# Optimization experiments

Hardware: AMD Instinct MI355X
Metric: run time of the kernel (lower is better)

Reference implementation:

```python
import jax, jax.numpy as jnp
import numpy as np

B, IN_DIM, UNITS, NUM_K, NUM_S = 4096, 128, 256, 64, 256


def setup_inputs() -> dict:
    key = jax.random.key(0)
    ks = jax.random.split(key, 24)
    d = {
        "X": jax.random.normal(ks[0], (B, IN_DIM), jnp.float32),
        "h_prev": jax.random.normal(ks[1], (B, UNITS), jnp.float32),
        "c_prev": jax.random.normal(ks[2], (B, UNITS), jnp.float32),
        "M_prev": jax.random.normal(ks[3], (B, NUM_K, NUM_S), jnp.float32),
        "k_prev": jax.random.normal(ks[4], (B, NUM_S), jnp.float32),
    }
    rows = IN_DIM + UNITS
    s = 0.05
    d["Wf"] = jax.random.normal(ks[5], (rows, UNITS), jnp.float32) * s
    d["Wt"] = jax.random.normal(ks[6], (rows, UNITS), jnp.float32) * s
    d["Wi"] = jax.random.normal(ks[7], (rows, UNITS), jnp.float32) * s
    d["Wo"] = jax.random.normal(ks[8], (rows, UNITS), jnp.float32) * s
    d["bf"] = jnp.zeros((UNITS,), jnp.float32)
    d["bt"] = jnp.zeros((UNITS,), jnp.float32)
    d["bi"] = jnp.zeros((UNITS,), jnp.float32)
    d["bo"] = jnp.zeros((UNITS,), jnp.float32)
    d["Wk"] = jax.random.normal(ks[9], (UNITS, NUM_S), jnp.float32) * s
    d["bk"] = jnp.zeros((NUM_S,), jnp.float32)
    d["Wr"] = jax.random.normal(ks[10], (NUM_S, UNITS), jnp.float32) * s
    d["Wc"] = jax.random.normal(ks[11], (UNITS, UNITS), jnp.float32) * s
    d["Wh"] = jax.random.normal(ks[12], (NUM_S, UNITS), jnp.float32) * s
    d["We"] = jax.random.normal(ks[13], (UNITS, NUM_S), jnp.float32) * s
    d["be"] = jnp.zeros((NUM_S,), jnp.float32)
    d["Wa"] = jax.random.normal(ks[14], (UNITS, NUM_S), jnp.float32) * s
    d["ba"] = jnp.zeros((NUM_S,), jnp.float32)
    return d


def _l2n(x):
    # matches tf.nn.l2_normalize: x / sqrt(max(sum(x^2), eps))
    return x / jnp.sqrt(jnp.maximum(jnp.sum(x * x, axis=-1, keepdims=True), 1e-12))


def reference(X, h_prev, c_prev, M_prev, k_prev,
              Wf, Wt, Wi, Wo, bf, bt, bi, bo,
              Wk, bk, Wr, Wc, Wh, We, be, Wa, ba):
    sig = jax.nn.sigmoid
    xh = jnp.concatenate([X, h_prev], axis=-1)          # (B, in+units)
    i = sig(xh @ Wi + bi)
    f = sig(xh @ Wf + bf)
    o = sig(xh @ Wo + bo)
    t = sig(xh @ Wt + bt)
    c = f * c_prev + i * t                              # (B, units)

    # tf.keras.losses.cosine_similarity returns NEGATIVE cosine similarity
    cos = jnp.einsum('bks,bs->bk', _l2n(M_prev), _l2n(k_prev))
    alpha = jax.nn.softmax(-cos, axis=-1)               # (B, K)
    r = jnp.einsum('bk,bks->bs', alpha, M_prev)         # content read (B, S)

    rc_1 = sig(r @ Wr + c @ Wc)
    h_curr = o * jnp.tanh(c + rc_1 * (r @ Wh))          # (B, units)

    k_curr = jnp.tanh(h_curr @ Wk + bk)                 # (B, S)
    e = sig(h_curr @ We + be)                           # erase  (B, S)
    a = jnp.tanh(h_curr @ Wa + ba)                      # add    (B, S)
    al = alpha[:, :, None]                              # (B, K, 1)
    M_curr = M_prev * (1.0 - al * e[:, None, :]) + al * a[:, None, :]
    return h_curr, c, M_curr, k_curr
```

## Files before the change

### kernel.cpp

```cpp
#include <hip/hip_runtime.h>
#include <math.h>


#define BATCH 4096
#define INDIM 128
#define UNITS 256
#define NUMK  64
#define NUMS  256

__device__ __forceinline__ float sigf(float x) { return 1.0f / (1.0f + expf(-x)); }

__global__ __launch_bounds__(256) void k1_gates(
    const float* __restrict__ X, const float* __restrict__ h_prev,
    const float* __restrict__ c_prev,
    const float* __restrict__ Wf, const float* __restrict__ Wt,
    const float* __restrict__ Wi, const float* __restrict__ Wo,
    const float* __restrict__ bf, const float* __restrict__ bt,
    const float* __restrict__ bi, const float* __restrict__ bo,
    float* __restrict__ c_out, float* __restrict__ o_out)
{
    __shared__ float sA[16][68];
    __shared__ float sB[4][16][68];

    const int t  = threadIdx.x;
    const int bm = blockIdx.x;
    const int bn = blockIdx.y;

    float acc[4][4][4];
    #pragma unroll
    for (int g = 0; g < 4; ++g)
        #pragma unroll
        for (int mi = 0; mi < 4; ++mi)
            #pragma unroll
            for (int ni = 0; ni < 4; ++ni) acc[g][mi][ni] = 0.0f;

    const float* Wg[4] = {Wf, Wt, Wi, Wo};

    const int m0 = (t & 15) * 4;
    const int n0 = (t >> 4) * 4;
    const int lm  = t >> 2;
    const int lk  = (t & 3) * 4;
    const int lbk = t >> 4;
    const int lbc = (t & 15) * 4;

    for (int k0 = 0; k0 < 384; k0 += 16) {
        {
            const int row = bm * 64 + lm;
            const int gk = k0 + lk;
            float4 av;
            if (gk < INDIM) av = *(const float4*)(X + row * INDIM + gk);
            else            av = *(const float4*)(h_prev + row * UNITS + (gk - INDIM));
            sA[lk + 0][lm] = av.x; sA[lk + 1][lm] = av.y;
            sA[lk + 2][lm] = av.z; sA[lk + 3][lm] = av.w;
        }
        #pragma unroll
        for (int g = 0; g < 4; ++g) {
            float4 bv = *(const float4*)(Wg[g] + (k0 + lbk) * UNITS + bn * 64 + lbc);
            *(float4*)&sB[g][lbk][lbc] = bv;
        }
        __syncthreads();
        #pragma unroll
        for (int k = 0; k < 16; ++k) {
            float a[4];
            *(float4*)a = *(float4*)&sA[k][m0];
            #pragma unroll
            for (int g = 0; g < 4; ++g) {
                float b[4];
                *(float4*)b = *(float4*)&sB[g][k][n0];
                #pragma unroll
                for (int mi = 0; mi < 4; ++mi)
                    #pragma unroll
                    for (int ni = 0; ni < 4; ++ni)
                        acc[g][mi][ni] = fmaf(a[mi], b[ni], acc[g][mi][ni]);
            }
        }
        __syncthreads();
    }

    const int col0 = bn * 64 + n0;
    const int row0 = bm * 64 + m0;
    float bfv[4], btv[4], biv[4], bov[4];
    *(float4*)bfv = *(const float4*)(bf + col0);
    *(float4*)btv = *(const float4*)(bt + col0);
    *(float4*)biv = *(const float4*)(bi + col0);
    *(float4*)bov = *(const float4*)(bo + col0);
    #pragma unroll
    for (int mi = 0; mi < 4; ++mi) {
        const int row = row0 + mi;
        float cp[4];
        *(float4*)cp = *(const float4*)(c_prev + row * UNITS + col0);
        float cv[4], ov[4];
        #pragma unroll
        for (int ni = 0; ni < 4; ++ni) {
            float fv = sigf(acc[0][mi][ni] + bfv[ni]);
            float tv = sigf(acc[1][mi][ni] + btv[ni]);
            float iv = sigf(acc[2][mi][ni] + biv[ni]);
            float oo = sigf(acc[3][mi][ni] + bov[ni]);
            cv[ni] = fv * cp[ni] + iv * tv;
            ov[ni] = oo;
        }
        *(float4*)(c_out + row * UNITS + col0) = *(float4*)cv;
        *(float4*)(o_out + row * UNITS + col0) = *(float4*)ov;
    }
}

__global__ __launch_bounds__(256) void k2_cosr(
    const float* __restrict__ M, const float* __restrict__ k_prev,
    float* __restrict__ alpha_out, float* __restrict__ r_out)
{
    const int b = blockIdx.x;
    const int t = threadIdx.x;
    const int lane = t & 63;
    const int w = t >> 6;

    __shared__ float scos[64];
    __shared__ float salpha[64];
    __shared__ float spr[4][256];

    const float4 k4 = *(const float4*)(k_prev + b * NUMS + lane * 4);
    float kss = k4.x * k4.x + k4.y * k4.y + k4.z * k4.z + k4.w * k4.w;
    #pragma unroll
    for (int m = 1; m < 64; m <<= 1) kss += __shfl_xor(kss, m, 64);
    const float knorm = sqrtf(fmaxf(kss, 1e-12f));

    const float* Mb = M + (size_t)b * (NUMK * NUMS);
    float4 mreg[16];
    #pragma unroll
    for (int j = 0; j < 16; ++j)
        mreg[j] = *(const float4*)(Mb + (w * 16 + j) * NUMS + lane * 4);

    #pragma unroll
    for (int j = 0; j < 16; ++j) {
        const float4 m4 = mreg[j];
        float dot = m4.x * k4.x + m4.y * k4.y + m4.z * k4.z + m4.w * k4.w;
        float ssq = m4.x * m4.x + m4.y * m4.y + m4.z * m4.z + m4.w * m4.w;
        #pragma unroll
        for (int m = 1; m < 64; m <<= 1) {
            dot += __shfl_xor(dot, m, 64);
            ssq += __shfl_xor(ssq, m, 64);
        }
        if (lane == 0) {
            const float mnorm = sqrtf(fmaxf(ssq, 1e-12f));
            scos[w * 16 + j] = dot / (mnorm * knorm);
        }
    }
    __syncthreads();

    if (t < 64) {
        float v = -scos[t];
        float vmax = v;
        #pragma unroll
        for (int m = 1; m < 64; m <<= 1) vmax = fmaxf(vmax, __shfl_xor(vmax, m, 64));
        float e = expf(v - vmax);
        float s = e;
        #pragma unroll
        for (int m = 1; m < 64; m <<= 1) s += __shfl_xor(s, m, 64);
        const float al = e / s;
        salpha[t] = al;
        alpha_out[b * NUMK + t] = al;
    }
    __syncthreads();

    float pr0 = 0.f, pr1 = 0.f, pr2 = 0.f, pr3 = 0.f;
    #pragma unroll
    for (int j = 0; j < 16; ++j) {
        const float al = salpha[w * 16 + j];
        pr0 = fmaf(al, mreg[j].x, pr0);
        pr1 = fmaf(al, mreg[j].y, pr1);
        pr2 = fmaf(al, mreg[j].z, pr2);
        pr3 = fmaf(al, mreg[j].w, pr3);
    }
    *(float4*)&spr[w][lane * 4] = make_float4(pr0, pr1, pr2, pr3);
    __syncthreads();
    const float rv = spr[0][t] + spr[1][t] + spr[2][t] + spr[3][t];
    r_out[b * NUMS + t] = rv;
}

__global__ __launch_bounds__(256) void k3_h(
    const float* __restrict__ r, const float* __restrict__ c,
    const float* __restrict__ o,
    const float* __restrict__ Wr, const float* __restrict__ Wc,
    const float* __restrict__ Wh,
    float* __restrict__ h_out)
{
    __shared__ float sAr[16][68];
    __shared__ float sAc[16][68];
    __shared__ float sB[3][16][68];

    const int t  = threadIdx.x;
    const int bm = blockIdx.x;
    const int bn = blockIdx.y;

    float acc[3][4][4];
    #pragma unroll
    for (int g = 0; g < 3; ++g)
        #pragma unroll
        for (int mi = 0; mi < 4; ++mi)
            #pragma unroll
            for (int ni = 0; ni < 4; ++ni) acc[g][mi][ni] = 0.0f;

    const float* Wg[3] = {Wr, Wc, Wh};
    const int m0 = (t & 15) * 4;
    const int n0 = (t >> 4) * 4;
    const int lm  = t >> 2;
    const int lk  = (t & 3) * 4;
    const int lbk = t >> 4;
    const int lbc = (t & 15) * 4;

    for (int k0 = 0; k0 < 256; k0 += 16) {
        {
            const int row = bm * 64 + lm;
            float4 rv = *(const float4*)(r + row * UNITS + k0 + lk);
            float4 cv = *(const float4*)(c + row * UNITS + k0 + lk);
            sAr[lk + 0][lm] = rv.x; sAr[lk + 1][lm] = rv.y;
            sAr[lk + 2][lm] = rv.z; sAr[lk + 3][lm] = rv.w;
            sAc[lk + 0][lm] = cv.x; sAc[lk + 1][lm] = cv.y;
            sAc[lk + 2][lm] = cv.z; sAc[lk + 3][lm] = cv.w;
        }
        #pragma unroll
        for (int g = 0; g < 3; ++g) {
            float4 bv = *(const float4*)(Wg[g] + (k0 + lbk) * UNITS + bn * 64 + lbc);
            *(float4*)&sB[g][lbk][lbc] = bv;
        }
        __syncthreads();
        #pragma unroll
        for (int k = 0; k < 16; ++k) {
            float ar[4], ac[4];
            *(float4*)ar = *(float4*)&sAr[k][m0];
            *(float4*)ac = *(float4*)&sAc[k][m0];
            float b0[4], b1[4], b2[4];
            *(float4*)b0 = *(float4*)&sB[0][k][n0];
            *(float4*)b1 = *(float4*)&sB[1][k][n0];
            *(float4*)b2 = *(float4*)&sB[2][k][n0];
            #pragma unroll
            for (int mi = 0; mi < 4; ++mi)
                #pragma unroll
                for (int ni = 0; ni < 4; ++ni) {
                    acc[0][mi][ni] = fmaf(ar[mi], b0[ni], acc[0][mi][ni]);
                    acc[1][mi][ni] = fmaf(ac[mi], b1[ni], acc[1][mi][ni]);
                    acc[2][mi][ni] = fmaf(ar[mi], b2[ni], acc[2][mi][ni]);
                }
        }
        __syncthreads();
    }

    const int col0 = bn * 64 + n0;
    const int row0 = bm * 64 + m0;
    #pragma unroll
    for (int mi = 0; mi < 4; ++mi) {
        const int row = row0 + mi;
        float cv[4], ov[4], hv[4];
        *(float4*)cv = *(const float4*)(c + row * UNITS + col0);
        *(float4*)ov = *(const float4*)(o + row * UNITS + col0);
        #pragma unroll
        for (int ni = 0; ni < 4; ++ni) {
            const float rc1 = sigf(acc[0][mi][ni] + acc[1][mi][ni]);
            hv[ni] = ov[ni] * tanhf(cv[ni] + rc1 * acc[2][mi][ni]);
        }
        *(float4*)(h_out + row * UNITS + col0) = *(float4*)hv;
    }
}

__global__ __launch_bounds__(256) void k4_kea(
    const float* __restrict__ h,
    const float* __restrict__ Wk, const float* __restrict__ We,
    const float* __restrict__ Wa,
    const float* __restrict__ bk, const float* __restrict__ be,
    const float* __restrict__ ba,
    float* __restrict__ k_out, float* __restrict__ e_out, float* __restrict__ a_out)
{
    __shared__ float sA[16][68];
    __shared__ float sB[3][16][68];

    const int t  = threadIdx.x;
    const int bm = blockIdx.x;
    const int bn = blockIdx.y;

    float acc[3][4][4];
    #pragma unroll
    for (int g = 0; g < 3; ++g)
        #pragma unroll
        for (int mi = 0; mi < 4; ++mi)
            #pragma unroll
            for (int ni = 0; ni < 4; ++ni) acc[g][mi][ni] = 0.0f;

    const float* Wg[3] = {Wk, We, Wa};
    const int m0 = (t & 15) * 4;
    const int n0 = (t >> 4) * 4;
    const int lm  = t >> 2;
    const int lk  = (t & 3) * 4;
    const int lbk = t >> 4;
    const int lbc = (t & 15) * 4;

    for (int k0 = 0; k0 < 256; k0 += 16) {
        {
            const int row = bm * 64 + lm;
            float4 av = *(const float4*)(h + row * UNITS + k0 + lk);
            sA[lk + 0][lm] = av.x; sA[lk + 1][lm] = av.y;
            sA[lk + 2][lm] = av.z; sA[lk + 3][lm] = av.w;
        }
        #pragma unroll
        for (int g = 0; g < 3; ++g) {
            float4 bv = *(const float4*)(Wg[g] + (k0 + lbk) * UNITS + bn * 64 + lbc);
            *(float4*)&sB[g][lbk][lbc] = bv;
        }
        __syncthreads();
        #pragma unroll
        for (int k = 0; k < 16; ++k) {
            float a[4];
            *(float4*)a = *(float4*)&sA[k][m0];
            float b0[4], b1[4], b2[4];
            *(float4*)b0 = *(float4*)&sB[0][k][n0];
            *(float4*)b1 = *(float4*)&sB[1][k][n0];
            *(float4*)b2 = *(float4*)&sB[2][k][n0];
            #pragma unroll
            for (int mi = 0; mi < 4; ++mi)
                #pragma unroll
                for (int ni = 0; ni < 4; ++ni) {
                    acc[0][mi][ni] = fmaf(a[mi], b0[ni], acc[0][mi][ni]);
                    acc[1][mi][ni] = fmaf(a[mi], b1[ni], acc[1][mi][ni]);
                    acc[2][mi][ni] = fmaf(a[mi], b2[ni], acc[2][mi][ni]);
                }
        }
        __syncthreads();
    }

    const int col0 = bn * 64 + n0;
    const int row0 = bm * 64 + m0;
    float bkv[4], bev[4], bav[4];
    *(float4*)bkv = *(const float4*)(bk + col0);
    *(float4*)bev = *(const float4*)(be + col0);
    *(float4*)bav = *(const float4*)(ba + col0);
    #pragma unroll
    for (int mi = 0; mi < 4; ++mi) {
        const int row = row0 + mi;
        float kv[4], ev[4], av[4];
        #pragma unroll
        for (int ni = 0; ni < 4; ++ni) {
            kv[ni] = tanhf(acc[0][mi][ni] + bkv[ni]);
            ev[ni] = sigf (acc[1][mi][ni] + bev[ni]);
            av[ni] = tanhf(acc[2][mi][ni] + bav[ni]);
        }
        *(float4*)(k_out + row * UNITS + col0) = *(float4*)kv;
        *(float4*)(e_out + row * UNITS + col0) = *(float4*)ev;
        *(float4*)(a_out + row * UNITS + col0) = *(float4*)av;
    }
}

__global__ __launch_bounds__(256) void k5_mup(
    const float* __restrict__ M, const float* __restrict__ alpha,
    const float* __restrict__ e, const float* __restrict__ a,
    float* __restrict__ Mout)
{
    const int b = blockIdx.x;
    const int t = threadIdx.x;
    __shared__ float sal[64];
    if (t < 64) sal[t] = alpha[b * NUMK + t];

    const int s4 = (t & 63) * 4;
    const int kr = t >> 6;
    const float4 e4 = *(const float4*)(e + b * NUMS + s4);
    const float4 a4 = *(const float4*)(a + b * NUMS + s4);
    __syncthreads();

    const float* Mb = M + (size_t)b * (NUMK * NUMS);
    float* Ob = Mout + (size_t)b * (NUMK * NUMS);
    #pragma unroll
    for (int j = 0; j < 16; ++j) {
        const int k = j * 4 + kr;
        const float al = sal[k];
        float4 m4 = *(const float4*)(Mb + k * NUMS + s4);
        float4 o4;
        o4.x = m4.x * (1.0f - al * e4.x) + al * a4.x;
        o4.y = m4.y * (1.0f - al * e4.y) + al * a4.y;
        o4.z = m4.z * (1.0f - al * e4.z) + al * a4.z;
        o4.w = m4.w * (1.0f - al * e4.w) + al * a4.w;
        *(float4*)(Ob + k * NUMS + s4) = o4;
    }
}

extern "C" void kernel_launch(void* const* d_in, const int* in_sizes, int n_in,
                              void* d_out, int out_size, void* d_ws, size_t ws_size,
                              hipStream_t stream)
{
    (void)in_sizes; (void)n_in; (void)out_size; (void)ws_size;

    const float* X      = (const float*)d_in[0];
    const float* h_prev = (const float*)d_in[1];
    const float* c_prev = (const float*)d_in[2];
    const float* M_prev = (const float*)d_in[3];
    const float* k_prev = (const float*)d_in[4];
    const float* Wf = (const float*)d_in[5];
    const float* Wt = (const float*)d_in[6];
    const float* Wi = (const float*)d_in[7];
    const float* Wo = (const float*)d_in[8];
    const float* bf = (const float*)d_in[9];
    const float* bt = (const float*)d_in[10];
    const float* bi = (const float*)d_in[11];
    const float* bo = (const float*)d_in[12];
    const float* Wk = (const float*)d_in[13];
    const float* bk = (const float*)d_in[14];
    const float* Wr = (const float*)d_in[15];
    const float* Wc = (const float*)d_in[16];
    const float* Wh = (const float*)d_in[17];
    const float* We = (const float*)d_in[18];
    const float* be = (const float*)d_in[19];
    const float* Wa = (const float*)d_in[20];
    const float* ba = (const float*)d_in[21];

    float* out = (float*)d_out;
    float* h_out = out;
    float* c_out = out + 1048576;
    float* M_out = out + 2097152;
    float* k_out = out + 69206016;

    float* ws    = (float*)d_ws;
    float* o_ws  = ws;
    float* al_ws = ws + 1048576;
    float* r_ws  = ws + 1310720;
    float* e_ws  = ws + 2359296;
    float* a_ws  = ws + 3407872;

    k1_gates<<<dim3(64, 4), 256, 0, stream>>>(X, h_prev, c_prev,
                                              Wf, Wt, Wi, Wo, bf, bt, bi, bo,
                                              c_out, o_ws);
    k2_cosr<<<dim3(4096), 256, 0, stream>>>(M_prev, k_prev, al_ws, r_ws);
    k3_h<<<dim3(64, 4), 256, 0, stream>>>(r_ws, c_out, o_ws, Wr, Wc, Wh, h_out);
    k4_kea<<<dim3(64, 4), 256, 0, stream>>>(h_out, Wk, We, Wa, bk, be, ba,
                                            k_out, e_ws, a_ws);
    k5_mup<<<dim3(4096), 256, 0, stream>>>(M_prev, al_ws, e_ws, a_ws, M_out);
}
```

Measured before the change: 720.7 us.

## Replace FP32 SIMT GEMMs with split-bf16 MFMA GEMMs plus elementwise epilogues

Replaces the three shared-memory FP32 FMA GEMM kernels with a generic MFMA GEMM that emulates FP32 precision using hi/lo bf16 splits (three MFMAs per tile). Weights and activations are packed into transposed bf16 hi/lo buffers by new pack and prep kernels, and gate nonlinearities move into separate elementwise kernels that also emit the next GEMM's split operands. The cosine reduction now uses partial shuffles plus shared-memory sums, and the large M reads and writes use nontemporal loads and stores. The cost is extra launches, weight repacking on every call, and large intermediate buffers written to and read back from global memory.

```diff
diff --git a/kernel.cpp b/kernel.cpp
--- a/kernel.cpp
+++ b/kernel.cpp
@@ -8,112 +8,208 @@
 #define NUMK  64
 #define NUMS  256
 
+typedef unsigned short u16;
+typedef __attribute__((ext_vector_type(4))) float  f32x4;
+typedef __attribute__((ext_vector_type(8))) short  s16x8;
+typedef __attribute__((ext_vector_type(4))) u16    u16x4;
+typedef __attribute__((ext_vector_type(8))) u16    u16x8;
+
 __device__ __forceinline__ float sigf(float x) { return 1.0f / (1.0f + expf(-x)); }
 
-__global__ __launch_bounds__(256) void k1_gates(
-    const float* __restrict__ X, const float* __restrict__ h_prev,
-    const float* __restrict__ c_prev,
+__device__ __forceinline__ u16 f2bf(float x) {
+    unsigned u = __float_as_uint(x);
+    return (u16)((u + 0x7fffu + ((u >> 16) & 1u)) >> 16);
+}
+__device__ __forceinline__ float bf2f(u16 h) {
+    return __uint_as_float(((unsigned)h) << 16);
+}
+__device__ __forceinline__ void split_bf(float x, u16& hi, u16& lo) {
+    hi = f2bf(x);
+    lo = f2bf(x - bf2f(hi));
+}
+
+__global__ __launch_bounds__(256) void prep_a1(
+    const float* __restrict__ X, const float* __restrict__ hp,
+    u16* __restrict__ Ahi, u16* __restrict__ Alo)
+{
+    const int idx = blockIdx.x * 256 + threadIdx.x;
+    const int row = idx / 96;
+    const int cg  = (idx - row * 96) * 4;
+    float4 v;
+    if (cg < INDIM) v = *(const float4*)(X + row * INDIM + cg);
+    else            v = *(const float4*)(hp + row * UNITS + (cg - INDIM));
+    u16x4 h, l;
+    u16 th, tl;
+    split_bf(v.x, th, tl); h.x = th; l.x = tl;
+    split_bf(v.y, th, tl); h.y = th; l.y = tl;
+    split_bf(v.z, th, tl); h.z = th; l.z = tl;
+    split_bf(v.w, th, tl); h.w = th; l.w = tl;
+    *(u16x4*)(Ahi + row * 384 + cg) = h;
+    *(u16x4*)(Alo + row * 384 + cg) = l;
+}
+
+__global__ __launch_bounds__(256) void pack_w1(
     const float* __restrict__ Wf, const float* __restrict__ Wt,
     const float* __restrict__ Wi, const float* __restrict__ Wo,
+    u16* __restrict__ Whi, u16* __restrict__ Wlo)
+{
+    const int tid = blockIdx.x * 256 + threadIdx.x;
+    const int n  = tid / 48;
+    const int k0 = (tid - n * 48) * 8;
+    const float* src = (n < 256) ? Wf : (n < 512) ? Wt : (n < 768) ? Wi : Wo;
+    const int nc = n & 255;
+    u16x8 h, l;
+    #pragma unroll
+    for (int j = 0; j < 8; ++j) {
+        float x = src[(k0 + j) * 256 + nc];
+        u16 th, tl;
+        split_bf(x, th, tl);
+        h[j] = th; l[j] = tl;
+    }
+    *(u16x8*)(Whi + n * 384 + k0) = h;
+    *(u16x8*)(Wlo + n * 384 + k0) = l;
+}
+
+__global__ __launch_bounds__(256) void pack_w3(
+    const float* __restrict__ Wr, const float* __restrict__ Wc,
+    const float* __restrict__ Wh,
+    u16* __restrict__ Whi, u16* __restrict__ Wlo)
+{
+    const int tid = blockIdx.x * 256 + threadIdx.x;
+    const int n  = tid / 64;
+    const int k0 = (tid - n * 64) * 8;
+    u16x8 h, l;
+    #pragma unroll
+    for (int j = 0; j < 8; ++j) {
+        const int k = k0 + j;
+        float x;
+        if (n < 256) x = (k < 256) ? Wr[k * 256 + n] : Wc[(k - 256) * 256 + n];
+        else         x = (k < 256) ? Wh[k * 256 + (n - 256)] : 0.0f;
+        u16 th, tl;
+        split_bf(x, th, tl);
+        h[j] = th; l[j] = tl;
+    }
+    *(u16x8*)(Whi + n * 512 + k0) = h;
+    *(u16x8*)(Wlo + n * 512 + k0) = l;
+}
+
+__global__ __launch_bounds__(256) void pack_w4(
+    const float* __restrict__ Wk, const float* __restrict__ We,
+    const float* __restrict__ Wa,
+    u16* __restrict__ Whi, u16* __restrict__ Wlo)
+{
+    const int tid = blockIdx.x * 256 + threadIdx.x;
+    const int n  = tid / 32;
+    const int k0 = (tid - n * 32) * 8;
+    const float* src = (n < 256) ? Wk : (n < 512) ? We : Wa;
+    const int nc = n & 255;
+    u16x8 h, l;
+    #pragma unroll
+    for (int j = 0; j < 8; ++j) {
+        float x = src[(k0 + j) * 256 + nc];
+        u16 th, tl;
+        split_bf(x, th, tl);
+        h[j] = th; l[j] = tl;
+    }
+    *(u16x8*)(Whi + n * 256 + k0) = h;
+    *(u16x8*)(Wlo + n * 256 + k0) = l;
+}
+
+template<int K>
+__global__ __launch_bounds__(256) void gemm_bf16x2(
+    const u16* __restrict__ Ahi, const u16* __restrict__ Alo,
+    const u16* __restrict__ Bhi, const u16* __restrict__ Blo,
+    float* __restrict__ C, int N)
+{
+    const int t = threadIdx.x;
+    const int wave = t >> 6, lane = t & 63;
+    const int m0 = blockIdx.x * 64 + wave * 16;
+    const int n0 = blockIdx.y * 64;
+    const int r = lane & 15, g = lane >> 4;
+
+    const u16* pAh = Ahi + (size_t)(m0 + r) * K + g * 8;
+    const u16* pAl = Alo + (size_t)(m0 + r) * K + g * 8;
+    const u16* pBh = Bhi + (size_t)(n0 + r) * K + g * 8;
+    const u16* pBl = Blo + (size_t)(n0 + r) * K + g * 8;
+
+    f32x4 acc[4];
+    #pragma unroll
+    for (int j = 0; j < 4; ++j) acc[j] = (f32x4){0.f, 0.f, 0.f, 0.f};
+
+    #pragma unroll 2
+    for (int k0 = 0; k0 < K; k0 += 32) {
+        s16x8 ah = *(const s16x8*)(pAh + k0);
+        s16x8 al = *(const s16x8*)(pAl + k0);
+        #pragma unroll
+        for (int j = 0; j < 4; ++j) {
+            s16x8 bh = *(const s16x8*)(pBh + (size_t)j * 16 * K + k0);
+            s16x8 bl = *(const s16x8*)(pBl + (size_t)j * 16 * K + k0);
+            acc[j] = __builtin_amdgcn_mfma_f32_16x16x32_bf16(ah, bh, acc[j], 0, 0, 0);
+            acc[j] = __builtin_amdgcn_mfma_f32_16x16x32_bf16(al, bh, acc[j], 0, 0, 0);
+            acc[j] = __builtin_amdgcn_mfma_f32_16x16x32_bf16(ah, bl, acc[j], 0, 0, 0);
+        }
+    }
+
+    #pragma unroll
+    for (int j = 0; j < 4; ++j)
+        #pragma unroll
+        for (int rr = 0; rr < 4; ++rr)
+            C[(size_t)(m0 + g * 4 + rr) * N + (n0 + j * 16 + r)] = acc[j][rr];
+}
+
+__global__ __launch_bounds__(256) void e1(
+    const float* __restrict__ G1, const float* __restrict__ c_prev,
     const float* __restrict__ bf, const float* __restrict__ bt,
     const float* __restrict__ bi, const float* __restrict__ bo,
-    float* __restrict__ c_out, float* __restrict__ o_out)
-{
-    __shared__ float sA[16][68];
-    __shared__ float sB[4][16][68];
-
-    const int t  = threadIdx.x;
-    const int bm = blockIdx.x;
-    const int bn = blockIdx.y;
-
-    float acc[4][4][4];
-    #pragma unroll
-    for (int g = 0; g < 4; ++g)
-        #pragma unroll
-        for (int mi = 0; mi < 4; ++mi)
-            #pragma unroll
-            for (int ni = 0; ni < 4; ++ni) acc[g][mi][ni] = 0.0f;
-
-    const float* Wg[4] = {Wf, Wt, Wi, Wo};
-
-    const int m0 = (t & 15) * 4;
-    const int n0 = (t >> 4) * 4;
-    const int lm  = t >> 2;
-    const int lk  = (t & 3) * 4;
-    const int lbk = t >> 4;
-    const int lbc = (t & 15) * 4;
-
-    for (int k0 = 0; k0 < 384; k0 += 16) {
-        {
-            const int row = bm * 64 + lm;
-            const int gk = k0 + lk;
-            float4 av;
-            if (gk < INDIM) av = *(const float4*)(X + row * INDIM + gk);
-            else            av = *(const float4*)(h_prev + row * UNITS + (gk - INDIM));
-            sA[lk + 0][lm] = av.x; sA[lk + 1][lm] = av.y;
-            sA[lk + 2][lm] = av.z; sA[lk + 3][lm] = av.w;
-        }
-        #pragma unroll
-        for (int g = 0; g < 4; ++g) {
-            float4 bv = *(const float4*)(Wg[g] + (k0 + lbk) * UNITS + bn * 64 + lbc);
-            *(float4*)&sB[g][lbk][lbc] = bv;
-        }
-        __syncthreads();
-        #pragma unroll
-        for (int k = 0; k < 16; ++k) {
-            float a[4];
-            *(float4*)a = *(float4*)&sA[k][m0];
-            #pragma unroll
-            for (int g = 0; g < 4; ++g) {
-                float b[4];
-                *(float4*)b = *(float4*)&sB[g][k][n0];
-                #pragma unroll
-                for (int mi = 0; mi < 4; ++mi)
-                    #pragma unroll
-                    for (int ni = 0; ni < 4; ++ni)
-                        acc[g][mi][ni] = fmaf(a[mi], b[ni], acc[g][mi][ni]);
-            }
-        }
-        __syncthreads();
-    }
-
-    const int col0 = bn * 64 + n0;
-    const int row0 = bm * 64 + m0;
-    float bfv[4], btv[4], biv[4], bov[4];
-    *(float4*)bfv = *(const float4*)(bf + col0);
-    *(float4*)btv = *(const float4*)(bt + col0);
-    *(float4*)biv = *(const float4*)(bi + col0);
-    *(float4*)bov = *(const float4*)(bo + col0);
-    #pragma unroll
-    for (int mi = 0; mi < 4; ++mi) {
-        const int row = row0 + mi;
-        float cp[4];
-        *(float4*)cp = *(const float4*)(c_prev + row * UNITS + col0);
-        float cv[4], ov[4];
-        #pragma unroll
-        for (int ni = 0; ni < 4; ++ni) {
-            float fv = sigf(acc[0][mi][ni] + bfv[ni]);
-            float tv = sigf(acc[1][mi][ni] + btv[ni]);
-            float iv = sigf(acc[2][mi][ni] + biv[ni]);
-            float oo = sigf(acc[3][mi][ni] + bov[ni]);
-            cv[ni] = fv * cp[ni] + iv * tv;
-            ov[ni] = oo;
-        }
-        *(float4*)(c_out + row * UNITS + col0) = *(float4*)cv;
-        *(float4*)(o_out + row * UNITS + col0) = *(float4*)ov;
-    }
+    float* __restrict__ c_out, u16* __restrict__ A3hi, u16* __restrict__ A3lo,
+    float* __restrict__ o_ws)
+{
+    const int idx = blockIdx.x * 256 + threadIdx.x;
+    const int row = idx >> 6;
+    const int c0  = (idx & 63) * 4;
+    const float* g = G1 + (size_t)row * 1024 + c0;
+    float4 fv = *(const float4*)(g);
+    float4 tv = *(const float4*)(g + 256);
+    float4 iv = *(const float4*)(g + 512);
+    float4 ov = *(const float4*)(g + 768);
+    float4 bfv = *(const float4*)(bf + c0), btv = *(const float4*)(bt + c0);
+    float4 biv = *(const float4*)(bi + c0), bov = *(const float4*)(bo + c0);
+    float4 cp = *(const float4*)(c_prev + (size_t)row * 256 + c0);
+    float fa[4] = {fv.x, fv.y, fv.z, fv.w}, ta[4] = {tv.x, tv.y, tv.z, tv.w};
+    float ia[4] = {iv.x, iv.y, iv.z, iv.w}, oa[4] = {ov.x, ov.y, ov.z, ov.w};
+    float ba_f[4] = {bfv.x, bfv.y, bfv.z, bfv.w}, ba_t[4] = {btv.x, btv.y, btv.z, btv.w};
+    float ba_i[4] = {biv.x, biv.y, biv.z, biv.w}, ba_o[4] = {bov.x, bov.y, bov.z, bov.w};
+    float cpa[4] = {cp.x, cp.y, cp.z, cp.w};
+    float cv[4], oo[4];
+    u16x4 chi, clo;
+    #pragma unroll
+    for (int j = 0; j < 4; ++j) {
+        float f = sigf(fa[j] + ba_f[j]);
+        float tt = sigf(ta[j] + ba_t[j]);
+        float i = sigf(ia[j] + ba_i[j]);
+        oo[j] = sigf(oa[j] + ba_o[j]);
+        cv[j] = f * cpa[j] + i * tt;
+        u16 th, tl;
+        split_bf(cv[j], th, tl);
+        chi[j] = th; clo[j] = tl;
+    }
+    *(float4*)(c_out + (size_t)row * 256 + c0) = make_float4(cv[0], cv[1], cv[2], cv[3]);
+    *(float4*)(o_ws + (size_t)row * 256 + c0) = make_float4(oo[0], oo[1], oo[2], oo[3]);
+    *(u16x4*)(A3hi + (size_t)row * 512 + 256 + c0) = chi;
+    *(u16x4*)(A3lo + (size_t)row * 512 + 256 + c0) = clo;
 }
 
 __global__ __launch_bounds__(256) void k2_cosr(
     const float* __restrict__ M, const float* __restrict__ k_prev,
-    float* __restrict__ alpha_out, float* __restrict__ r_out)
+    float* __restrict__ alpha_out, u16* __restrict__ A3hi, u16* __restrict__ A3lo)
 {
     const int b = blockIdx.x;
     const int t = threadIdx.x;
     const int lane = t & 63;
     const int w = t >> 6;
 
-    __shared__ float scos[64];
+    __shared__ float sdot[64][8];
+    __shared__ float sssq[64][8];
     __shared__ float salpha[64];
     __shared__ float spr[4][256];
 
@@ -124,30 +220,34 @@
     const float knorm = sqrtf(fmaxf(kss, 1e-12f));
 
     const float* Mb = M + (size_t)b * (NUMK * NUMS);
-    float4 mreg[16];
+    f32x4 mreg[16];
     #pragma unroll
     for (int j = 0; j < 16; ++j)
-        mreg[j] = *(const float4*)(Mb + (w * 16 + j) * NUMS + lane * 4);
+        mreg[j] = __builtin_nontemporal_load((const f32x4*)(Mb + (w * 16 + j) * NUMS + lane * 4));
 
     #pragma unroll
     for (int j = 0; j < 16; ++j) {
-        const float4 m4 = mreg[j];
+        const f32x4 m4 = mreg[j];
         float dot = m4.x * k4.x + m4.y * k4.y + m4.z * k4.z + m4.w * k4.w;
         float ssq = m4.x * m4.x + m4.y * m4.y + m4.z * m4.z + m4.w * m4.w;
         #pragma unroll
-        for (int m = 1; m < 64; m <<= 1) {
+        for (int m = 1; m < 8; m <<= 1) {
             dot += __shfl_xor(dot, m, 64);
             ssq += __shfl_xor(ssq, m, 64);
         }
-        if (lane == 0) {
-            const float mnorm = sqrtf(fmaxf(ssq, 1e-12f));
-            scos[w * 16 + j] = dot / (mnorm * knorm);
+        if ((lane & 7) == 0) {
+            sdot[w * 16 + j][lane >> 3] = dot;
+            sssq[w * 16 + j][lane >> 3] = ssq;
         }
     }
     __syncthreads();
 
     if (t < 64) {
-        float v = -scos[t];
+        float dot = 0.f, ssq = 0.f;
+        #pragma unroll
+        for (int q = 0; q < 8; ++q) { dot += sdot[t][q]; ssq += sssq[t][q]; }
+        const float cosv = dot / (sqrtf(fmaxf(ssq, 1e-12f)) * knorm);
+        float v = -cosv;
         float vmax = v;
         #pragma unroll
         for (int m = 1; m < 64; m <<= 1) vmax = fmaxf(vmax, __shfl_xor(vmax, m, 64));
@@ -173,178 +273,69 @@
     *(float4*)&spr[w][lane * 4] = make_float4(pr0, pr1, pr2, pr3);
     __syncthreads();
     const float rv = spr[0][t] + spr[1][t] + spr[2][t] + spr[3][t];
-    r_out[b * NUMS + t] = rv;
-}
-
-__global__ __launch_bounds__(256) void k3_h(
-    const float* __restrict__ r, const float* __restrict__ c,
+    u16 hi, lo;
+    split_bf(rv, hi, lo);
+    A3hi[(size_t)b * 512 + t] = hi;
+    A3lo[(size_t)b * 512 + t] = lo;
+}
+
+__global__ __launch_bounds__(256) void e2(
+    const float* __restrict__ G3, const float* __restrict__ c,
     const float* __restrict__ o,
-    const float* __restrict__ Wr, const float* __restrict__ Wc,
-    const float* __restrict__ Wh,
-    float* __restrict__ h_out)
-{
-    __shared__ float sAr[16][68];
-    __shared__ float sAc[16][68];
-    __shared__ float sB[3][16][68];
-
-    const int t  = threadIdx.x;
-    const int bm = blockIdx.x;
-    const int bn = blockIdx.y;
-
-    float acc[3][4][4];
-    #pragma unroll
-    for (int g = 0; g < 3; ++g)
-        #pragma unroll
-        for (int mi = 0; mi < 4; ++mi)
-            #pragma unroll
-            for (int ni = 0; ni < 4; ++ni) acc[g][mi][ni] = 0.0f;
-
-    const float* Wg[3] = {Wr, Wc, Wh};
-    const int m0 = (t & 15) * 4;
-    const int n0 = (t >> 4) * 4;
-    const int lm  = t >> 2;
-    const int lk  = (t & 3) * 4;
-    const int lbk = t >> 4;
-    const int lbc = (t & 15) * 4;
-
-    for (int k0 = 0; k0 < 256; k0 += 16) {
-        {
-            const int row = bm * 64 + lm;
-            float4 rv = *(const float4*)(r + row * UNITS + k0 + lk);
-            float4 cv = *(const float4*)(c + row * UNITS + k0 + lk);
-            sAr[lk + 0][lm] = rv.x; sAr[lk + 1][lm] = rv.y;
-            sAr[lk + 2][lm] = rv.z; sAr[lk + 3][lm] = rv.w;
-            sAc[lk + 0][lm] = cv.x; sAc[lk + 1][lm] = cv.y;
-            sAc[lk + 2][lm] = cv.z; sAc[lk + 3][lm] = cv.w;
-        }
-        #pragma unroll
-        for (int g = 0; g < 3; ++g) {
-            float4 bv = *(const float4*)(Wg[g] + (k0 + lbk) * UNITS + bn * 64 + lbc);
-            *(float4*)&sB[g][lbk][lbc] = bv;
-        }
-        __syncthreads();
-        #pragma unroll
-        for (int k = 0; k < 16; ++k) {
-            float ar[4], ac[4];
-            *(float4*)ar = *(float4*)&sAr[k][m0];
-            *(float4*)ac = *(float4*)&sAc[k][m0];
-            float b0[4], b1[4], b2[4];
-            *(float4*)b0 = *(float4*)&sB[0][k][n0];
-            *(float4*)b1 = *(float4*)&sB[1][k][n0];
-            *(float4*)b2 = *(float4*)&sB[2][k][n0];
-            #pragma unroll
-            for (int mi = 0; mi < 4; ++mi)
-                #pragma unroll
-                for (int ni = 0; ni < 4; ++ni) {
-                    acc[0][mi][ni] = fmaf(ar[mi], b0[ni], acc[0][mi][ni]);
-                    acc[1][mi][ni] = fmaf(ac[mi], b1[ni], acc[1][mi][ni]);
-                    acc[2][mi][ni] = fmaf(ar[mi], b2[ni], acc[2][mi][ni]);
-                }
-        }
-        __syncthreads();
-    }
-
-    const int col0 = bn * 64 + n0;
-    const int row0 = bm * 64 + m0;
-    #pragma unroll
-    for (int mi = 0; mi < 4; ++mi) {
-        const int row = row0 + mi;
-        float cv[4], ov[4], hv[4];
-        *(float4*)cv = *(const float4*)(c + row * UNITS + col0);
-        *(float4*)ov = *(const float4*)(o + row * UNITS + col0);
-        #pragma unroll
-        for (int ni = 0; ni < 4; ++ni) {
-            const float rc1 = sigf(acc[0][mi][ni] + acc[1][mi][ni]);
-            hv[ni] = ov[ni] * tanhf(cv[ni] + rc1 * acc[2][mi][ni]);
-        }
-        *(float4*)(h_out + row * UNITS + col0) = *(float4*)hv;
-    }
-}
-
-__global__ __launch_bounds__(256) void k4_kea(
-    const float* __restrict__ h,
-    const float* __restrict__ Wk, const float* __restrict__ We,
-    const float* __restrict__ Wa,
+    float* __restrict__ h_out, u16* __restrict__ A4hi, u16* __restrict__ A4lo)
+{
+    const int idx = blockIdx.x * 256 + threadIdx.x;
+    const int row = idx >> 6;
+    const int c0  = (idx & 63) * 4;
+    float4 rc = *(const float4*)(G3 + (size_t)row * 512 + c0);
+    float4 rh = *(const float4*)(G3 + (size_t)row * 512 + 256 + c0);
+    float4 cv = *(const float4*)(c + (size_t)row * 256 + c0);
+    float4 ov = *(const float4*)(o + (size_t)row * 256 + c0);
+    float rca[4] = {rc.x, rc.y, rc.z, rc.w}, rha[4] = {rh.x, rh.y, rh.z, rh.w};
+    float ca[4] = {cv.x, cv.y, cv.z, cv.w}, oa[4] = {ov.x, ov.y, ov.z, ov.w};
+    float hv[4];
+    u16x4 hhi, hlo;
+    #pragma unroll
+    for (int j = 0; j < 4; ++j) {
+        hv[j] = oa[j] * tanhf(ca[j] + sigf(rca[j]) * rha[j]);
+        u16 th, tl;
+        split_bf(hv[j], th, tl);
+        hhi[j] = th; hlo[j] = tl;
+    }
+    *(float4*)(h_out + (size_t)row * 256 + c0) = make_float4(hv[0], hv[1], hv[2], hv[3]);
+    *(u16x4*)(A4hi + (size_t)row * 256 + c0) = hhi;
+    *(u16x4*)(A4lo + (size_t)row * 256 + c0) = hlo;
+}
+
+__global__ __launch_bounds__(256) void e3(
+    const float* __restrict__ G4,
     const float* __restrict__ bk, const float* __restrict__ be,
     const float* __restrict__ ba,
-    float* __restrict__ k_out, float* __restrict__ e_out, float* __restrict__ a_out)
-{
-    __shared__ float sA[16][68];
-    __shared__ float sB[3][16][68];
-
-    const int t  = threadIdx.x;
-    const int bm = blockIdx.x;
-    const int bn = blockIdx.y;
-
-    float acc[3][4][4];
-    #pragma unroll
-    for (int g = 0; g < 3; ++g)
-        #pragma unroll
-        for (int mi = 0; mi < 4; ++mi)
-            #pragma unroll
-            for (int ni = 0; ni < 4; ++ni) acc[g][mi][ni] = 0.0f;
-
-    const float* Wg[3] = {Wk, We, Wa};
-    const int m0 = (t & 15) * 4;
-    const int n0 = (t >> 4) * 4;
-    const int lm  = t >> 2;
-    const int lk  = (t & 3) * 4;
-    const int lbk = t >> 4;
-    const int lbc = (t & 15) * 4;
-
-    for (int k0 = 0; k0 < 256; k0 += 16) {
-        {
-            const int row = bm * 64 + lm;
-            float4 av = *(const float4*)(h + row * UNITS + k0 + lk);
-            sA[lk + 0][lm] = av.x; sA[lk + 1][lm] = av.y;
-            sA[lk + 2][lm] = av.z; sA[lk + 3][lm] = av.w;
-        }
-        #pragma unroll
-        for (int g = 0; g < 3; ++g) {
-            float4 bv = *(const float4*)(Wg[g] + (k0 + lbk) * UNITS + bn * 64 + lbc);
-            *(float4*)&sB[g][lbk][lbc] = bv;
-        }
-        __syncthreads();
-        #pragma unroll
-        for (int k = 0; k < 16; ++k) {
-            float a[4];
-            *(float4*)a = *(float4*)&sA[k][m0];
-            float b0[4], b1[4], b2[4];
-            *(float4*)b0 = *(float4*)&sB[0][k][n0];
-            *(float4*)b1 = *(float4*)&sB[1][k][n0];
-            *(float4*)b2 = *(float4*)&sB[2][k][n0];
-            #pragma unroll
-            for (int mi = 0; mi < 4; ++mi)
-                #pragma unroll
-                for (int ni = 0; ni < 4; ++ni) {
-                    acc[0][mi][ni] = fmaf(a[mi], b0[ni], acc[0][mi][ni]);
-                    acc[1][mi][ni] = fmaf(a[mi], b1[ni], acc[1][mi][ni]);
-                    acc[2][mi][ni] = fmaf(a[mi], b2[ni], acc[2][mi][ni]);
-                }
-        }
-        __syncthreads();
-    }
-
-    const int col0 = bn * 64 + n0;
-    const int row0 = bm * 64 + m0;
-    float bkv[4], bev[4], bav[4];
-    *(float4*)bkv = *(const float4*)(bk + col0);
-    *(float4*)bev = *(const float4*)(be + col0);
-    *(float4*)bav = *(const float4*)(ba + col0);
-    #pragma unroll
-    for (int mi = 0; mi < 4; ++mi) {
-        const int row = row0 + mi;
-        float kv[4], ev[4], av[4];
-        #pragma unroll
-        for (int ni = 0; ni < 4; ++ni) {
-            kv[ni] = tanhf(acc[0][mi][ni] + bkv[ni]);
-            ev[ni] = sigf (acc[1][mi][ni] + bev[ni]);
-            av[ni] = tanhf(acc[2][mi][ni] + bav[ni]);
-        }
-        *(float4*)(k_out + row * UNITS + col0) = *(float4*)kv;
-        *(float4*)(e_out + row * UNITS + col0) = *(float4*)ev;
-        *(float4*)(a_out + row * UNITS + col0) = *(float4*)av;
-    }
+    float* __restrict__ k_out, float* __restrict__ e_ws, float* __restrict__ a_ws)
+{
+    const int idx = blockIdx.x * 256 + threadIdx.x;
+    const int row = idx >> 6;
+    const int c0  = (idx & 63) * 4;
+    const float* g = G4 + (size_t)row * 768 + c0;
+    float4 kv = *(const float4*)(g);
+    float4 ev = *(const float4*)(g + 256);
+    float4 av = *(const float4*)(g + 512);
+    float4 bkv = *(const float4*)(bk + c0), bev = *(const float4*)(be + c0);
+    float4 bav = *(const float4*)(ba + c0);
+    float ka[4] = {kv.x, kv.y, kv.z, kv.w}, ea[4] = {ev.x, ev.y, ev.z, ev.w};
+    float aa[4] = {av.x, av.y, av.z, av.w};
+    float bka[4] = {bkv.x, bkv.y, bkv.z, bkv.w}, bea[4] = {bev.x, bev.y, bev.z, bev.w};
+    float baa[4] = {bav.x, bav.y, bav.z, bav.w};
+    float ko[4], eo[4], ao[4];
+    #pragma unroll
+    for (int j = 0; j < 4; ++j) {
+        ko[j] = tanhf(ka[j] + bka[j]);
+        eo[j] = sigf (ea[j] + bea[j]);
+        ao[j] = tanhf(aa[j] + baa[j]);
+    }
+    *(float4*)(k_out + (size_t)row * 256 + c0) = make_float4(ko[0], ko[1], ko[2], ko[3]);
+    *(float4*)(e_ws  + (size_t)row * 256 + c0) = make_float4(eo[0], eo[1], eo[2], eo[3]);
+    *(float4*)(a_ws  + (size_t)row * 256 + c0) = make_float4(ao[0], ao[1], ao[2], ao[3]);
 }
 
 __global__ __launch_bounds__(256) void k5_mup(
@@ -369,13 +360,13 @@
     for (int j = 0; j < 16; ++j) {
         const int k = j * 4 + kr;
         const float al = sal[k];
-        float4 m4 = *(const float4*)(Mb + k * NUMS + s4);
-        float4 o4;
+        f32x4 m4 = __builtin_nontemporal_load((const f32x4*)(Mb + k * NUMS + s4));
+        f32x4 o4;
         o4.x = m4.x * (1.0f - al * e4.x) + al * a4.x;
         o4.y = m4.y * (1.0f - al * e4.y) + al * a4.y;
         o4.z = m4.z * (1.0f - al * e4.z) + al * a4.z;
         o4.w = m4.w * (1.0f - al * e4.w) + al * a4.w;
-        *(float4*)(Ob + k * NUMS + s4) = o4;
+        __builtin_nontemporal_store(o4, (f32x4*)(Ob + k * NUMS + s4));
     }
 }
 
@@ -414,19 +405,44 @@
     float* M_out = out + 2097152;
     float* k_out = out + 69206016;
 
-    float* ws    = (float*)d_ws;
-    float* o_ws  = ws;
-    float* al_ws = ws + 1048576;
-    float* r_ws  = ws + 1310720;
-    float* e_ws  = ws + 2359296;
-    float* a_ws  = ws + 3407872;
-
-    k1_gates<<<dim3(64, 4), 256, 0, stream>>>(X, h_prev, c_prev,
-                                              Wf, Wt, Wi, Wo, bf, bt, bi, bo,
-                                              c_out, o_ws);
-    k2_cosr<<<dim3(4096), 256, 0, stream>>>(M_prev, k_prev, al_ws, r_ws);
-    k3_h<<<dim3(64, 4), 256, 0, stream>>>(r_ws, c_out, o_ws, Wr, Wc, Wh, h_out);
-    k4_kea<<<dim3(64, 4), 256, 0, stream>>>(h_out, Wk, We, Wa, bk, be, ba,
-                                            k_out, e_ws, a_ws);
-    k5_mup<<<dim3(4096), 256, 0, stream>>>(M_prev, al_ws, e_ws, a_ws, M_out);
-}
+    char* w = (char*)d_ws;
+    size_t off = 0;
+    auto carve = [&](size_t bytes) { void* p = w + off; off += (bytes + 255) & ~(size_t)255; return p; };
+    u16* A1hi = (u16*)carve(4096ull * 384 * 2);
+    u16* A1lo = (u16*)carve(4096ull * 384 * 2);
+    u16* W1hi = (u16*)carve(1024ull * 384 * 2);
+    u16* W1lo = (u16*)carve(1024ull * 384 * 2);
+    u16* W3hi = (u16*)carve(512ull * 512 * 2);
+    u16* W3lo = (u16*)carve(512ull * 512 * 2);
+    u16* W4hi = (u16*)carve(768ull * 256 * 2);
+    u16* W4lo = (u16*)carve(768ull * 256 * 2);
+    u16* A3hi = (u16*)carve(4096ull * 512 * 2);
+    u16* A3lo = (u16*)carve(4096ull * 512 * 2);
+    u16* A4hi = (u16*)carve(4096ull * 256 * 2);
+    u16* A4lo = (u16*)carve(4096ull * 256 * 2);
+    float* G1  = (float*)carve(4096ull * 1024 * 4);
+    float* G3  = (float*)carve(4096ull * 512 * 4);
+    float* G4  = (float*)carve(4096ull * 768 * 4);
+    float* o_ws  = (float*)carve(4096ull * 256 * 4);
+    float* al_ws = (float*)carve(4096ull * 64 * 4);
+    float* e_ws  = (float*)carve(4096ull * 256 * 4);
+    float* a_ws  = (float*)carve(4096ull * 256 * 4);
+
+    pack_w1<<<192, 256, 0, stream>>>(Wf, Wt, Wi, Wo, W1hi, W1lo);
+    pack_w3<<<128, 256, 0, stream>>>(Wr, Wc, Wh, W3hi, W3lo);
+    pack_w4<<<96, 256, 0, stream>>>(Wk, We, Wa, W4hi, W4lo);
+    prep_a1<<<1536, 256, 0, stream>>>(X, h_prev, A1hi, A1lo);
+
+    k2_cosr<<<4096, 256, 0, stream>>>(M_prev, k_prev, al_ws, A3hi, A3lo);
+
+    gemm_bf16x2<384><<<dim3(64, 16), 256, 0, stream>>>(A1hi, A1lo, W1hi, W1lo, G1, 1024);
+    e1<<<1024, 256, 0, stream>>>(G1, c_prev, bf, bt, bi, bo, c_out, A3hi, A3lo, o_ws);
+
+    gemm_bf16x2<512><<<dim3(64, 8), 256, 0, stream>>>(A3hi, A3lo, W3hi, W3lo, G3, 512);
+    e2<<<1024, 256, 0, stream>>>(G3, c_out, o_ws, h_out, A4hi, A4lo);
+
+    gemm_bf16x2<256><<<dim3(64, 12), 256, 0, stream>>>(A4hi, A4lo, W4hi, W4lo, G4, 768);
+    e3<<<1024, 256, 0, stream>>>(G4, bk, be, ba, k_out, e_ws, a_ws);
+
+    k5_mup<<<4096, 256, 0, stream>>>(M_prev, al_ws, e_ws, a_ws, M_out);
+}
```

Result: faster. 681.3 us (-5.5%).
